# Kernel tuning notes

Measured on AMD Instinct MI355X. Metric: run time of the kernel, lower is better.

## Reference

```python
import jax, jax.numpy as jnp
import numpy as np

B, S, D = 16, 1024, 512
H, DH = 8, 64  # heads, dim_head


def setup_inputs() -> dict:
    key = jax.random.key(0)
    ks = jax.random.split(key, 7)
    x = jax.random.normal(ks[0], (B, S, D), dtype=jnp.float32)
    # variable sequence lengths in [1, S]
    seq_lens = jnp.maximum(jax.random.randint(ks[1], (B,), 0, S + 1), 1).astype(jnp.int32)
    w_std = 0.02
    Wq = jax.random.normal(ks[2], (D, D), dtype=jnp.float32) * w_std
    Wk = jax.random.normal(ks[3], (D, D), dtype=jnp.float32) * w_std
    Wv = jax.random.normal(ks[4], (D, D), dtype=jnp.float32) * w_std
    Wo = jax.random.normal(ks[5], (D, D), dtype=jnp.float32) * w_std
    bo = jnp.zeros((D,), dtype=jnp.float32)
    return {"x": x, "seq_lens": seq_lens, "Wq": Wq, "Wk": Wk, "Wv": Wv, "Wo": Wo, "bo": bo}


def reference(x, seq_lens, Wq, Wk, Wv, Wo, bo):
    # x: [B, S, D] padded ragged batch; seq_lens: [B] valid token counts.
    # Equivalent to the per-batch SDPA loop over jagged sequences: attention
    # is computed only among the valid tokens of each sequence.
    scale = DH ** -0.5
    q = (x @ Wq).reshape(B, S, H, DH)
    k = (x @ Wk).reshape(B, S, H, DH)
    v = (x @ Wv).reshape(B, S, H, DH)
    scores = jnp.einsum('bqhd,bkhd->bhqk', q, k) * scale  # [B,H,S,S]
    valid = jnp.arange(S)[None, :] < seq_lens[:, None]     # [B,S] token mask
    neg_inf = jnp.finfo(scores.dtype).min
    scores = jnp.where(valid[:, None, None, :], scores, neg_inf)
    attn = jax.nn.softmax(scores, axis=-1)
    out = jnp.einsum('bhqk,bkhd->bqhd', attn, v).reshape(B, S, D)
    out = out @ Wo + bo  # to_out Linear (dropout=0 / eval)
    return out * valid[:, :, None]  # zero padded query positions
```

## Files before the change

### kernel.cpp

```cpp
#include <hip/hip_runtime.h>
#include <hip/hip_bf16.h>

typedef __bf16 bf16_t;
typedef __attribute__((ext_vector_type(4))) __bf16 bf16x4;
typedef __attribute__((ext_vector_type(8))) __bf16 bf16x8;
typedef __attribute__((ext_vector_type(4))) float f32x4;

#define MFMA16(a, b, c) __builtin_amdgcn_mfma_f32_16x16x32_bf16((a), (b), (c), 0, 0, 0)

#define BB 16
#define SS 1024
#define DD 512
#define HH 8
#define DH 64
#define NTOK (BB * SS)
#define QSCALE 0.18033688f

typedef const __attribute__((address_space(1))) void gas_void;
typedef __attribute__((address_space(3))) void las_void;

__device__ __forceinline__ void async_cp16(const void* g, void* l) {
    __builtin_amdgcn_global_load_lds((gas_void*)g, (las_void*)l, 16, 0, 0);
}

__device__ __forceinline__ bf16x8 frag_ld(const char* sm, int row, int kk, int g) {
    int r7 = row & 7;
    int base = row * 128 + ((g & 1) << 3);
    int c0 = ((kk << 2) + (g >> 1)) ^ r7;
    int c1 = ((kk << 2) + 2 + (g >> 1)) ^ r7;
    bf16x4 lo = *(const bf16x4*)(sm + base + (c0 << 4));
    bf16x4 hi = *(const bf16x4*)(sm + base + (c1 << 4));
    return __builtin_shufflevector(lo, hi, 0, 1, 2, 3, 4, 5, 6, 7);
}

__device__ __forceinline__ bf16x8 fragl(const char* sm, int idx, int l) {
    return *(const bf16x8*)(sm + (idx * 64 + l) * 16);
}

__global__ __launch_bounds__(256) void cast_x_k(const float* __restrict__ x,
                                                bf16_t* __restrict__ xb, int n4) {
    int i = blockIdx.x * 256 + threadIdx.x;
    if (i < n4) {
        float4 v = ((const float4*)x)[i];
        bf16x4 o;
        o[0] = (bf16_t)v.x; o[1] = (bf16_t)v.y; o[2] = (bf16_t)v.z; o[3] = (bf16_t)v.w;
        *(bf16x4*)(xb + (size_t)i * 4) = o;
    }
}

__global__ __launch_bounds__(256) void transpose_w_k(const float* __restrict__ W0,
                                                     const float* __restrict__ W1,
                                                     const float* __restrict__ W2,
                                                     const float* __restrict__ W3,
                                                     bf16_t* __restrict__ Wt) {
    __shared__ float t[32][33];
    int z = blockIdx.z;
    const float* W = (z == 0) ? W0 : (z == 1) ? W1 : (z == 2) ? W2 : W3;
    bf16_t* out = Wt + (size_t)z * DD * DD;
    int n0 = blockIdx.x * 32, k0 = blockIdx.y * 32;
    int tx = threadIdx.x, ty = threadIdx.y;
#pragma unroll
    for (int i = 0; i < 32; i += 8)
        t[ty + i][tx] = W[(size_t)(k0 + ty + i) * DD + n0 + tx];
    __syncthreads();
#pragma unroll
    for (int i = 0; i < 32; i += 8)
        out[(size_t)(n0 + ty + i) * DD + k0 + tx] = (bf16_t)t[tx][ty + i];
}

__global__ void build_q_k(const int* __restrict__ sl, ushort* __restrict__ items,
                          int* __restrict__ meta) {
    int l = threadIdx.x;
    __shared__ int s_b[BB], s_cnt[BB], s_start[BB];
    if (l < BB) {
        int len = sl[l];
        int rank = 0;
        for (int j = 0; j < BB; ++j) {
            int lj = sl[j];
            if (lj > len || (lj == len && j < l)) ++rank;
        }
        s_b[rank] = l;
        s_cnt[rank] = ((len + 63) >> 6) * HH;
    }
    __syncthreads();
    if (l < BB) {
        int st = 0;
        for (int j = 0; j < l; ++j) st += s_cnt[j];
        s_start[l] = st;
        if (l == BB - 1) { meta[0] = st + s_cnt[l]; meta[1] = 0; }
    }
    __syncthreads();
    if (l < BB) {
        int b = s_b[l], st = s_start[l], c = s_cnt[l];
        int nq = c >> 3;
        for (int i = 0; i < c; ++i) {
            int h = i / nq, qt = i - h * nq;
            items[st + i] = (ushort)((((b << 3) | h) << 4) | qt);
        }
    }
}

template <int MODE>
__global__ __launch_bounds__(256) void gemm_k(const bf16_t* __restrict__ A,
                                              const bf16_t* __restrict__ WtBase,
                                              bf16_t* __restrict__ oQ,
                                              bf16_t* __restrict__ oK,
                                              bf16_t* __restrict__ oVt,
                                              float* __restrict__ oO,
                                              const float* __restrict__ bo,
                                              const int* __restrict__ seq_lens) {
    __shared__ __align__(16) char smem[32768];
    char* smA = smem;
    char* smB = smem + 16384;
    const int tid = threadIdx.x;
    const int l = tid & 63, w = tid >> 6;
    const int lr = l & 15, g = l >> 4;
    const int bm = blockIdx.x, bn = blockIdx.y;
    const int z = (MODE == 0) ? blockIdx.z : 3;
    const bf16_t* Wt = WtBase + (size_t)z * DD * DD;
    const int row0 = bm * 128;
    const int col0 = bn * 128;
    const int wm = (w >> 1) * 64, wn = (w & 1) * 64;

    f32x4 acc[4][4] = {};

    for (int kt = 0; kt < 8; ++kt) {
        const int k0 = kt * 64;
        __syncthreads();
#pragma unroll
        for (int it = 0; it < 4; ++it) {
            int cl = it * 256 + tid;
            int m = cl >> 3, p = cl & 7, c = p ^ (m & 7);
            async_cp16(A + (size_t)(row0 + m) * DD + k0 + c * 8, smA + cl * 16);
        }
#pragma unroll
        for (int it = 0; it < 4; ++it) {
            int cl = it * 256 + tid;
            int m = cl >> 3, p = cl & 7, c = p ^ (m & 7);
            async_cp16(Wt + (size_t)(col0 + m) * DD + k0 + c * 8, smB + cl * 16);
        }
        __syncthreads();
#pragma unroll
        for (int kk = 0; kk < 2; ++kk) {
            bf16x8 af[4], bfr[4];
#pragma unroll
            for (int i = 0; i < 4; ++i) af[i] = frag_ld(smA, wm + i * 16 + lr, kk, g);
#pragma unroll
            for (int j = 0; j < 4; ++j) bfr[j] = frag_ld(smB, wn + j * 16 + lr, kk, g);
#pragma unroll
            for (int i = 0; i < 4; ++i)
#pragma unroll
                for (int j = 0; j < 4; ++j)
                    acc[i][j] = MFMA16(af[i], bfr[j], acc[i][j]);
        }
    }

    if (MODE == 0) {
        __syncthreads();
        char* tl = smem;
        const float sc = (z == 0) ? QSCALE : 1.f;
#pragma unroll
        for (int i = 0; i < 4; ++i)
#pragma unroll
            for (int j = 0; j < 4; ++j)
#pragma unroll
                for (int r = 0; r < 4; ++r) {
                    int s = wm + i * 16 + g * 4 + r;
                    int n = wn + j * 16 + lr;
                    int nb = 2 * n;
                    int byte = s * 256 + ((((nb >> 4) ^ (s & 7)) << 4) | (nb & 15));
                    *(bf16_t*)(tl + byte) = (bf16_t)(acc[i][j][r] * sc);
                }
        __syncthreads();
        const int b = row0 >> 10, s0 = row0 & 1023;
        if (z < 2) {
            bf16_t* dst = (z == 0) ? oQ : oK;
#pragma unroll
            for (int c8 = 0; c8 < 8; ++c8) {
                int combo = c8 * 4 + w;
                int kk = combo & 1, t = (combo >> 1) & 7, hl = combo >> 4;
                int s = 16 * t + lr;
                bf16x4 pr[2];
#pragma unroll
                for (int jj = 0; jj < 2; ++jj) {
                    int nb = 128 * hl + 64 * kk + 32 * jj + 8 * g;
                    int byte = s * 256 + ((((nb >> 4) ^ (s & 7)) << 4) | (nb & 15));
                    pr[jj] = *(const bf16x4*)(tl + byte);
                }
                bf16x8 v = __builtin_shufflevector(pr[0], pr[1], 0, 1, 2, 3, 4, 5, 6, 7);
                int bhh = b * 8 + (col0 >> 6) + hl;
                int tg = (s0 >> 4) + t;
                *(bf16x8*)(dst + (((size_t)bhh * 64 + tg) * 2 + kk) * 512 + l * 8) = v;
            }
        } else {
#pragma unroll
            for (int c8 = 0; c8 < 8; ++c8) {
                int combo = c8 * 4 + w;
                int kk = combo & 1, dt = (combo >> 1) & 3;
                int st = (combo >> 3) & 1, hl = (combo >> 4) & 1;
                bf16x8 v;
#pragma unroll
                for (int j = 0; j < 8; ++j) {
                    int s = 64 * st + 32 * kk + 16 * (j >> 2) + 4 * g + (j & 3);
                    int n = 64 * hl + 16 * dt + lr;
                    int nb = 2 * n;
                    int byte = s * 256 + ((((nb >> 4) ^ (s & 7)) << 4) | (nb & 15));
                    v[j] = *(const bf16_t*)(tl + byte);
                }
                int bhh = b * 8 + (col0 >> 6) + hl;
                int stg = (s0 >> 6) + st;
                *(bf16x8*)(oVt + ((((size_t)bhh * 16 + stg) * 4 + dt) * 2 + kk) * 512 +
                           l * 8) = v;
            }
        }
    } else {
        int b = row0 >> 10;
        int len = seq_lens[b];
#pragma unroll
        for (int i = 0; i < 4; ++i) {
            int mrow = row0 + wm + i * 16 + g * 4;
#pragma unroll
            for (int j = 0; j < 4; ++j) {
                int n = col0 + wn + j * 16 + lr;
                float bias = bo[n];
#pragma unroll
                for (int r = 0; r < 4; ++r) {
                    int m = mrow + r;
                    int s = m & 1023;
                    oO[(size_t)m * DD + n] = (s < len) ? (acc[i][j][r] + bias) : 0.f;
                }
            }
        }
    }
}

__global__ __launch_bounds__(256) void attn_k(const bf16_t* __restrict__ Qf,
                                              const bf16_t* __restrict__ Kf,
                                              const bf16_t* __restrict__ Vf,
                                              bf16_t* __restrict__ O,
                                              const int* __restrict__ seq_lens,
                                              const ushort* __restrict__ items,
                                              int* __restrict__ meta) {
    __shared__ __align__(16) char smem[32768];
    __shared__ int s_item;
    const int tid = threadIdx.x, l = tid & 63, w = tid >> 6;
    const int lr = l & 15, g = l >> 4;
    const int nitems = meta[0];
    int* cursor = meta + 1;

    for (;;) {
        if (tid == 0) s_item = atomicAdd(cursor, 1);
        __syncthreads();
        const int ii = s_item;
        if (ii >= nitems) return;
        const int itv = items[ii];
        const int qt = itv & 15, bh = itv >> 4;
        const int b = bh >> 3, h = bh & 7;
        const int len = seq_lens[b];
        const int q0 = qt * 64 + w * 16;

        const bf16_t* kfb = Kf + (size_t)bh * 65536;
        const bf16_t* vfb = Vf + (size_t)bh * 65536;

        bf16x8 bq[2];
        {
            size_t tb = ((size_t)bh * 64 + (q0 >> 4)) * 2;
            bq[0] = *(const bf16x8*)(Qf + (tb + 0) * 512 + l * 8);
            bq[1] = *(const bf16x8*)(Qf + (tb + 1) * 512 + l * 8);
        }

        f32x4 oacc[4] = {};
        float mrun = -1e30f, lpart = 0.f;

        const int nkt = (len + 63) >> 6;

        auto stage = [&](int buf, int kti) {
            char* smK = smem + buf * 16384;
            char* smV = smK + 8192;
            const bf16_t* ks = kfb + kti * 4096;
            const bf16_t* vs = vfb + kti * 4096;
            async_cp16(ks + tid * 8, smK + tid * 16);
            async_cp16(ks + (256 + tid) * 8, smK + (256 + tid) * 16);
            async_cp16(vs + tid * 8, smV + tid * 16);
            async_cp16(vs + (256 + tid) * 8, smV + (256 + tid) * 16);
        };

        stage(0, 0);
        int cur = 0;

        for (int kt = 0; kt < nkt; ++kt) {
            const int key0 = kt * 64;
            asm volatile("s_waitcnt vmcnt(0)" ::: "memory");
            __builtin_amdgcn_s_barrier();
            if (kt + 1 < nkt) stage(cur ^ 1, kt + 1);
            const char* smK = smem + cur * 16384;
            const char* smV = smK + 8192;

            f32x4 pacc[4] = {};
#pragma unroll
            for (int nt = 0; nt < 4; ++nt) {
                bf16x8 ak0 = fragl(smK, nt * 2 + 0, l);
                bf16x8 ak1 = fragl(smK, nt * 2 + 1, l);
                pacc[nt] = MFMA16(ak0, bq[0], pacc[nt]);
                pacc[nt] = MFMA16(ak1, bq[1], pacc[nt]);
            }

            const bool full = (key0 + 64 <= len);

            float mloc = -1e30f;
            if (full) {
#pragma unroll
                for (int nt = 0; nt < 4; ++nt)
#pragma unroll
                    for (int r = 0; r < 4; ++r) mloc = fmaxf(mloc, pacc[nt][r]);
            } else {
#pragma unroll
                for (int nt = 0; nt < 4; ++nt)
#pragma unroll
                    for (int r = 0; r < 4; ++r) {
                        int kg = key0 + nt * 16 + 4 * g + r;
                        float s = (kg < len) ? pacc[nt][r] : -1e30f;
                        pacc[nt][r] = s;
                        mloc = fmaxf(mloc, s);
                    }
            }
            mloc = fmaxf(mloc, __shfl_xor(mloc, 16, 64));
            mloc = fmaxf(mloc, __shfl_xor(mloc, 32, 64));

            if (!__all(mloc <= mrun + 8.f)) {
                float mn = fmaxf(mrun, mloc);
                float corr = __builtin_amdgcn_exp2f(mrun - mn);
                mrun = mn;
                lpart *= corr;
                float cb[4];
#pragma unroll
                for (int r = 0; r < 4; ++r) cb[r] = __shfl(corr, 4 * g + r, 64);
#pragma unroll
                for (int dt = 0; dt < 4; ++dt)
#pragma unroll
                    for (int r = 0; r < 4; ++r) oacc[dt][r] *= cb[r];
            }

            float ls = 0.f;
#pragma unroll
            for (int nt = 0; nt < 4; ++nt)
#pragma unroll
                for (int r = 0; r < 4; ++r) {
                    float p = __builtin_amdgcn_exp2f(pacc[nt][r] - mrun);
                    pacc[nt][r] = p;
                    ls += p;
                }
            lpart += ls;

            bf16x8 pa[2];
#pragma unroll
            for (int kf = 0; kf < 2; ++kf)
#pragma unroll
                for (int j = 0; j < 8; ++j)
                    pa[kf][j] = (bf16_t)pacc[2 * kf + (j >> 2)][j & 3];
#pragma unroll
            for (int kf = 0; kf < 2; ++kf)
#pragma unroll
                for (int dt = 0; dt < 4; ++dt) {
                    bf16x8 bv = fragl(smV, dt * 2 + kf, l);
                    oacc[dt] = MFMA16(pa[kf], bv, oacc[dt]);
                }
            cur ^= 1;
        }

        {
            float lt = lpart;
            lt += __shfl_xor(lt, 16, 64);
            lt += __shfl_xor(lt, 32, 64);
#pragma unroll
            for (int r = 0; r < 4; ++r) {
                float inv = 1.f / __shfl(lt, 4 * g + r, 64);
                int q = q0 + 4 * g + r;
                size_t orow = ((size_t)b * SS + q) * DD;
#pragma unroll
                for (int dt = 0; dt < 4; ++dt)
                    O[orow + h * DH + dt * 16 + lr] = (bf16_t)(oacc[dt][r] * inv);
            }
        }
    }
}

extern "C" void kernel_launch(void* const* d_in, const int* in_sizes, int n_in,
                              void* d_out, int out_size, void* d_ws, size_t ws_size,
                              hipStream_t stream) {
    const float* x = (const float*)d_in[0];
    const int* seq_lens = (const int*)d_in[1];
    const float* Wq = (const float*)d_in[2];
    const float* Wk = (const float*)d_in[3];
    const float* Wv = (const float*)d_in[4];
    const float* Wo = (const float*)d_in[5];
    const float* bo = (const float*)d_in[6];
    float* out = (float*)d_out;

    char* ws = (char*)d_ws;
    const size_t SEG = (size_t)NTOK * DD * sizeof(bf16_t);
    bf16_t* xb = (bf16_t*)ws;
    bf16_t* qb = (bf16_t*)(ws + SEG);
    bf16_t* kb = (bf16_t*)(ws + 2 * SEG);
    bf16_t* vtb = (bf16_t*)(ws + 3 * SEG);
    bf16_t* wt = (bf16_t*)(ws + 4 * SEG);
    ushort* items = (ushort*)(ws + 4 * SEG + (size_t)4 * DD * DD * sizeof(bf16_t));
    int* meta = (int*)(items + 4096);
    bf16_t* ab = xb;

    build_q_k<<<dim3(1), dim3(64), 0, stream>>>(seq_lens, items, meta);
    cast_x_k<<<dim3((NTOK * DD / 4) / 256), dim3(256), 0, stream>>>(x, xb, NTOK * DD / 4);
    transpose_w_k<<<dim3(16, 16, 4), dim3(32, 8), 0, stream>>>(Wq, Wk, Wv, Wo, wt);
    gemm_k<0><<<dim3(NTOK / 128, DD / 128, 3), dim3(256), 0, stream>>>(
        xb, wt, qb, kb, vtb, nullptr, nullptr, nullptr);
    attn_k<<<dim3(1280), dim3(256), 0, stream>>>(qb, kb, vtb, ab, seq_lens, items, meta);
    gemm_k<2><<<dim3(NTOK / 128, DD / 128, 1), dim3(256), 0, stream>>>(
        ab, wt, nullptr, nullptr, nullptr, out, bo, seq_lens);
}
```

Measured before the change: 126.4 us.

## Split attention over key chunks with a separate combine kernel

Each (batch, head, query-tile) work item is split into chunks of up to four 64-key tiles. Every chunk writes an unnormalized partial output plus its running max and sum, and a new combine kernel merges the chunks with log-sum-exp weighting. This is meant to balance work across CUs and shorten the long serial key loops for long sequences. In exchange it adds partial-output traffic to workspace, an extra kernel launch, and a bf16 rounding of partial results. The split only activates when the workspace is large enough.

New measurement: 183.5 us. +45.2%, slower.

```diff
diff --git a/kernel.cpp b/kernel.cpp
--- a/kernel.cpp
+++ b/kernel.cpp
@@ -69,7 +69,7 @@
 }
 
 __global__ void build_q_k(const int* __restrict__ sl, ushort* __restrict__ items,
-                          int* __restrict__ meta) {
+                          int* __restrict__ meta, int split) {
     int l = threadIdx.x;
     __shared__ int s_b[BB], s_cnt[BB], s_start[BB];
     if (l < BB) {
@@ -80,7 +80,9 @@
             if (lj > len || (lj == len && j < l)) ++rank;
         }
         s_b[rank] = l;
-        s_cnt[rank] = ((len + 63) >> 6) * HH;
+        int nq = (len + 63) >> 6;
+        int nc = split ? ((len + 255) >> 8) : 1;
+        s_cnt[rank] = HH * nq * nc;
     }
     __syncthreads();
     if (l < BB) {
@@ -91,11 +93,14 @@
     }
     __syncthreads();
     if (l < BB) {
-        int b = s_b[l], st = s_start[l], c = s_cnt[l];
-        int nq = c >> 3;
-        for (int i = 0; i < c; ++i) {
-            int h = i / nq, qt = i - h * nq;
-            items[st + i] = (ushort)((((b << 3) | h) << 4) | qt);
+        int b = s_b[l], st = s_start[l], cnt = s_cnt[l];
+        int len = sl[b];
+        int nq = (len + 63) >> 6;
+        for (int i = 0; i < cnt; ++i) {
+            int qt = i % nq;
+            int ch = i / nq;
+            int h = ch & 7, cc = ch >> 3;
+            items[st + i] = (ushort)(((((b * 8 + h) << 4) | qt) << 2) | cc);
         }
     }
 }
@@ -238,9 +243,11 @@
                                               const bf16_t* __restrict__ Kf,
                                               const bf16_t* __restrict__ Vf,
                                               bf16_t* __restrict__ O,
+                                              bf16_t* __restrict__ pO,
+                                              float2* __restrict__ ml,
                                               const int* __restrict__ seq_lens,
                                               const ushort* __restrict__ items,
-                                              int* __restrict__ meta) {
+                                              int* __restrict__ meta, int split) {
     __shared__ __align__(16) char smem[32768];
     __shared__ int s_item;
     const int tid = threadIdx.x, l = tid & 63, w = tid >> 6;
@@ -254,10 +261,14 @@
         const int ii = s_item;
         if (ii >= nitems) return;
         const int itv = items[ii];
-        const int qt = itv & 15, bh = itv >> 4;
+        const int cc = itv & 3, qt = (itv >> 2) & 15, bh = itv >> 6;
         const int b = bh >> 3, h = bh & 7;
         const int len = seq_lens[b];
         const int q0 = qt * 64 + w * 16;
+        const int nkt = (len + 63) >> 6;
+        const int nc = split ? ((len + 255) >> 8) : 1;
+        const int kt0 = split ? cc * 4 : 0;
+        const int kt1 = split ? min(kt0 + 4, nkt) : nkt;
 
         const bf16_t* kfb = Kf + (size_t)bh * 65536;
         const bf16_t* vfb = Vf + (size_t)bh * 65536;
@@ -271,8 +282,6 @@
 
         f32x4 oacc[4] = {};
         float mrun = -1e30f, lpart = 0.f;
-
-        const int nkt = (len + 63) >> 6;
 
         auto stage = [&](int buf, int kti) {
             char* smK = smem + buf * 16384;
@@ -285,14 +294,14 @@
             async_cp16(vs + (256 + tid) * 8, smV + (256 + tid) * 16);
         };
 
-        stage(0, 0);
+        stage(0, kt0);
         int cur = 0;
 
-        for (int kt = 0; kt < nkt; ++kt) {
+        for (int kt = kt0; kt < kt1; ++kt) {
             const int key0 = kt * 64;
             asm volatile("s_waitcnt vmcnt(0)" ::: "memory");
             __builtin_amdgcn_s_barrier();
-            if (kt + 1 < nkt) stage(cur ^ 1, kt + 1);
+            if (kt + 1 < kt1) stage(cur ^ 1, kt + 1);
             const char* smK = smem + cur * 16384;
             const char* smV = smK + 8192;
 
@@ -368,10 +377,10 @@
             cur ^= 1;
         }
 
-        {
-            float lt = lpart;
-            lt += __shfl_xor(lt, 16, 64);
-            lt += __shfl_xor(lt, 32, 64);
+        float lt = lpart;
+        lt += __shfl_xor(lt, 16, 64);
+        lt += __shfl_xor(lt, 32, 64);
+        if (nc == 1) {
 #pragma unroll
             for (int r = 0; r < 4; ++r) {
                 float inv = 1.f / __shfl(lt, 4 * g + r, 64);
@@ -381,8 +390,72 @@
                 for (int dt = 0; dt < 4; ++dt)
                     O[orow + h * DH + dt * 16 + lr] = (bf16_t)(oacc[dt][r] * inv);
             }
-        }
-    }
+        } else {
+            bf16_t* pdst = pO + ((size_t)(cc * 128 + bh) * SS + q0) * DH;
+#pragma unroll
+            for (int r = 0; r < 4; ++r) {
+                int q = 4 * g + r;
+#pragma unroll
+                for (int dt = 0; dt < 4; ++dt)
+                    pdst[(size_t)q * DH + dt * 16 + lr] = (bf16_t)oacc[dt][r];
+            }
+            if (l < 16) {
+                float2 v;
+                v.x = mrun;
+                v.y = lt;
+                ml[(size_t)(cc * 128 + bh) * SS + q0 + l] = v;
+            }
+        }
+    }
+}
+
+__global__ __launch_bounds__(256) void combine_k(const bf16_t* __restrict__ pO,
+                                                 const float2* __restrict__ ml,
+                                                 bf16_t* __restrict__ ab,
+                                                 const int* __restrict__ sl) {
+    const int bid = blockIdx.x;
+    const int rb = bid & 31, h = (bid >> 5) & 7, b = bid >> 8;
+    const int len = sl[b];
+    const int nc = (len + 255) >> 8;
+    if (nc < 2) return;
+    const int tid = threadIdx.x;
+    const int row = rb * 32 + (tid >> 3);
+    const int dh0 = (tid & 7) * 8;
+    const int bh = b * 8 + h;
+
+    float m[4], lv[4];
+    float M = -1e30f;
+#pragma unroll
+    for (int c = 0; c < 4; ++c) {
+        if (c < nc) {
+            float2 v = ml[(size_t)(c * 128 + bh) * SS + row];
+            m[c] = v.x; lv[c] = v.y;
+            M = fmaxf(M, v.x);
+        } else {
+            m[c] = -1e30f; lv[c] = 0.f;
+        }
+    }
+    float L = 0.f, wgt[4];
+#pragma unroll
+    for (int c = 0; c < 4; ++c) {
+        wgt[c] = __builtin_amdgcn_exp2f(m[c] - M);
+        L += lv[c] * wgt[c];
+    }
+    const float invL = 1.f / L;
+    float acc[8] = {};
+#pragma unroll
+    for (int c = 0; c < 4; ++c) {
+        if (c < nc) {
+            bf16x8 p = *(const bf16x8*)(pO + ((size_t)(c * 128 + bh) * SS + row) * DH +
+                                        dh0);
+#pragma unroll
+            for (int j = 0; j < 8; ++j) acc[j] += wgt[c] * (float)p[j];
+        }
+    }
+    bf16x8 o;
+#pragma unroll
+    for (int j = 0; j < 8; ++j) o[j] = (bf16_t)(acc[j] * invL);
+    *(bf16x8*)(ab + ((size_t)b * SS + row) * DD + h * DH + dh0) = o;
 }
 
 extern "C" void kernel_launch(void* const* d_in, const int* in_sizes, int n_in,
@@ -404,16 +477,26 @@
     bf16_t* kb = (bf16_t*)(ws + 2 * SEG);
     bf16_t* vtb = (bf16_t*)(ws + 3 * SEG);
     bf16_t* wt = (bf16_t*)(ws + 4 * SEG);
-    ushort* items = (ushort*)(ws + 4 * SEG + (size_t)4 * DD * DD * sizeof(bf16_t));
-    int* meta = (int*)(items + 4096);
+    const size_t WT_BYTES = (size_t)4 * DD * DD * sizeof(bf16_t);
+    ushort* items = (ushort*)(ws + 4 * SEG + WT_BYTES);
+    int* meta = (int*)(items + 8192);
+    char* pbase = ws + 4 * SEG + WT_BYTES + 32768;
+    bf16_t* pO = (bf16_t*)pbase;
+    float2* mlp = (float2*)(pbase + (size_t)4 * 128 * SS * DH * 2);
+    const size_t NEED = 4 * SEG + WT_BYTES + 32768 +
+                        (size_t)4 * 128 * SS * DH * 2 + (size_t)4 * 128 * SS * 8;
+    const int split = (ws_size >= NEED) ? 1 : 0;
     bf16_t* ab = xb;
 
-    build_q_k<<<dim3(1), dim3(64), 0, stream>>>(seq_lens, items, meta);
+    build_q_k<<<dim3(1), dim3(64), 0, stream>>>(seq_lens, items, meta, split);
     cast_x_k<<<dim3((NTOK * DD / 4) / 256), dim3(256), 0, stream>>>(x, xb, NTOK * DD / 4);
     transpose_w_k<<<dim3(16, 16, 4), dim3(32, 8), 0, stream>>>(Wq, Wk, Wv, Wo, wt);
     gemm_k<0><<<dim3(NTOK / 128, DD / 128, 3), dim3(256), 0, stream>>>(
         xb, wt, qb, kb, vtb, nullptr, nullptr, nullptr);
-    attn_k<<<dim3(1280), dim3(256), 0, stream>>>(qb, kb, vtb, ab, seq_lens, items, meta);
+    attn_k<<<dim3(1280), dim3(256), 0, stream>>>(qb, kb, vtb, ab, pO, mlp, seq_lens,
+                                                 items, meta, split);
+    if (split)
+        combine_k<<<dim3(BB * HH * 32), dim3(256), 0, stream>>>(pO, mlp, ab, seq_lens);
     gemm_k<2><<<dim3(NTOK / 128, DD / 128, 1), dim3(256), 0, stream>>>(
         ab, wt, nullptr, nullptr, nullptr, out, bo, seq_lens);
 }
```

## Skip GEMM tiles beyond sequence length and prioritize MFMA waves in attention

Applied to the files above, without the earlier changes.

The QKV projection GEMM now returns early for 128-row tiles that lie wholly past the 64-rounded valid length, and the output GEMM writes zeros directly for fully padded tiles without doing the matmul. Fully valid output tiles also skip the per-element mask check. In the attention kernel, s_setprio raises wave priority around the MFMA blocks to improve overlap with other waves. Skipped Q/K/V regions stay uninitialized, which is safe only if attention never reads keys or queries beyond the rounded length.

New measurement: 129.0 us. +2.0%, slower.

```diff
diff --git a/kernel.cpp b/kernel.cpp
--- a/kernel.cpp
+++ b/kernel.cpp
@@ -122,6 +122,28 @@
     const int col0 = bn * 128;
     const int wm = (w >> 1) * 64, wn = (w & 1) * 64;
 
+    const int bb = row0 >> 10, s0 = row0 & 1023;
+    const int len = seq_lens[bb];
+
+    if (MODE == 0) {
+        if (s0 >= ((len + 63) & ~63)) return;
+    } else {
+        if (s0 >= len) {
+#pragma unroll
+            for (int i = 0; i < 4; ++i) {
+                int mrow = row0 + wm + i * 16 + g * 4;
+#pragma unroll
+                for (int j = 0; j < 4; ++j) {
+                    int n = col0 + wn + j * 16 + lr;
+#pragma unroll
+                    for (int r = 0; r < 4; ++r)
+                        oO[(size_t)(mrow + r) * DD + n] = 0.f;
+                }
+            }
+            return;
+        }
+    }
+
     f32x4 acc[4][4] = {};
 
     for (int kt = 0; kt < 8; ++kt) {
@@ -172,7 +194,7 @@
                     *(bf16_t*)(tl + byte) = (bf16_t)(acc[i][j][r] * sc);
                 }
         __syncthreads();
-        const int b = row0 >> 10, s0 = row0 & 1023;
+        const int b = bb;
         if (z < 2) {
             bf16_t* dst = (z == 0) ? oQ : oK;
 #pragma unroll
@@ -214,8 +236,7 @@
             }
         }
     } else {
-        int b = row0 >> 10;
-        int len = seq_lens[b];
+        const bool fullv = (s0 + 128 <= len);
 #pragma unroll
         for (int i = 0; i < 4; ++i) {
             int mrow = row0 + wm + i * 16 + g * 4;
@@ -223,11 +244,17 @@
             for (int j = 0; j < 4; ++j) {
                 int n = col0 + wn + j * 16 + lr;
                 float bias = bo[n];
-#pragma unroll
-                for (int r = 0; r < 4; ++r) {
-                    int m = mrow + r;
-                    int s = m & 1023;
-                    oO[(size_t)m * DD + n] = (s < len) ? (acc[i][j][r] + bias) : 0.f;
+                if (fullv) {
+#pragma unroll
+                    for (int r = 0; r < 4; ++r)
+                        oO[(size_t)(mrow + r) * DD + n] = acc[i][j][r] + bias;
+                } else {
+#pragma unroll
+                    for (int r = 0; r < 4; ++r) {
+                        int m = mrow + r;
+                        int s = m & 1023;
+                        oO[(size_t)m * DD + n] = (s < len) ? (acc[i][j][r] + bias) : 0.f;
+                    }
                 }
             }
         }
@@ -297,6 +324,7 @@
             const char* smV = smK + 8192;
 
             f32x4 pacc[4] = {};
+            __builtin_amdgcn_s_setprio(1);
 #pragma unroll
             for (int nt = 0; nt < 4; ++nt) {
                 bf16x8 ak0 = fragl(smK, nt * 2 + 0, l);
@@ -304,6 +332,7 @@
                 pacc[nt] = MFMA16(ak0, bq[0], pacc[nt]);
                 pacc[nt] = MFMA16(ak1, bq[1], pacc[nt]);
             }
+            __builtin_amdgcn_s_setprio(0);
 
             const bool full = (key0 + 64 <= len);
 
@@ -358,6 +387,7 @@
 #pragma unroll
                 for (int j = 0; j < 8; ++j)
                     pa[kf][j] = (bf16_t)pacc[2 * kf + (j >> 2)][j & 3];
+            __builtin_amdgcn_s_setprio(1);
 #pragma unroll
             for (int kf = 0; kf < 2; ++kf)
 #pragma unroll
@@ -365,6 +395,7 @@
                     bf16x8 bv = fragl(smV, dt * 2 + kf, l);
                     oacc[dt] = MFMA16(pa[kf], bv, oacc[dt]);
                 }
+            __builtin_amdgcn_s_setprio(0);
             cur ^= 1;
         }
 
@@ -412,7 +443,7 @@
     cast_x_k<<<dim3((NTOK * DD / 4) / 256), dim3(256), 0, stream>>>(x, xb, NTOK * DD / 4);
     transpose_w_k<<<dim3(16, 16, 4), dim3(32, 8), 0, stream>>>(Wq, Wk, Wv, Wo, wt);
     gemm_k<0><<<dim3(NTOK / 128, DD / 128, 3), dim3(256), 0, stream>>>(
-        xb, wt, qb, kb, vtb, nullptr, nullptr, nullptr);
+        xb, wt, qb, kb, vtb, nullptr, nullptr, seq_lens);
     attn_k<<<dim3(1280), dim3(256), 0, stream>>>(qb, kb, vtb, ab, seq_lens, items, meta);
     gemm_k<2><<<dim3(NTOK / 128, DD / 128, 1), dim3(256), 0, stream>>>(
         ab, wt, nullptr, nullptr, nullptr, out, bo, seq_lens);
```
